# Performance work log

Measured on AMD Instinct MI355X. Metric: run time of the kernel, lower is better.

Reference implementation:

```python
import jax, jax.numpy as jnp
import numpy as np

NUM_USER = 200000
NUM_ITEM = 100000
DIM = 64
NUM_LAYER = 2  # hardcoded in LightGCN.__init__ (lgn_single(..., num_layer=2))
AVG_DEG = 16
N = NUM_USER + NUM_ITEM
E = N * AVG_DEG
BATCH = 16384


def setup_inputs() -> dict:
    key = jax.random.key(0)
    k = jax.random.split(key, 8)
    emb_user = jax.random.normal(k[0], (NUM_USER, DIM), jnp.float32) * 0.05
    emb_item = jax.random.normal(k[1], (NUM_ITEM, DIM), jnp.float32) * 0.05
    # COO sparse normalized adjacency: out[row] += vals * x[col]
    graph_row = jax.random.randint(k[2], (E,), 0, N, dtype=jnp.int32)
    graph_col = jax.random.randint(k[3], (E,), 0, N, dtype=jnp.int32)
    graph_vals = jax.random.uniform(k[4], (E,), jnp.float32) / AVG_DEG
    user_nodes = jax.random.randint(k[5], (BATCH,), 0, NUM_USER, dtype=jnp.int32)
    pos_item_nodes = jax.random.randint(k[6], (BATCH,), 0, NUM_ITEM, dtype=jnp.int32) + NUM_USER
    neg_item_nodes = jax.random.randint(k[7], (BATCH,), 0, NUM_ITEM, dtype=jnp.int32) + NUM_USER
    return {
        "emb_user": emb_user,
        "emb_item": emb_item,
        "graph_vals": graph_vals,
        "graph_row": graph_row,
        "graph_col": graph_col,
        "user_nodes": user_nodes,
        "pos_item_nodes": pos_item_nodes,
        "neg_item_nodes": neg_item_nodes,
    }


def _spmm(vals, row, col, x):
    # torch.sparse.mm(graph, x) with graph in COO form
    return jax.ops.segment_sum(vals[:, None] * x[col], row, num_segments=N)


def reference(emb_user, emb_item, graph_vals, graph_row, graph_col,
              user_nodes, pos_item_nodes, neg_item_nodes):
    # LGN_single.forward: concat, propagate, mean over layer stack
    all_emb = jnp.concatenate([emb_user, emb_item], axis=0)  # [N, D]
    acc = all_emb
    e = all_emb
    for _ in range(NUM_LAYER):
        e = _spmm(graph_vals, graph_row, graph_col, e)
        acc = acc + e
    light_out = acc / (NUM_LAYER + 1)  # mean of stacked embeddings
    # LightGCN.forward: gather + elementwise dot scores
    u = light_out[user_nodes]          # [B, D]
    p = light_out[pos_item_nodes]      # [B, D]
    n = light_out[neg_item_nodes]      # [B, D]
    pos_scores = jnp.sum(u * p, axis=1)
    neg_scores = jnp.sum(u * n, axis=1)
    return jnp.stack([pos_scores, neg_scores])  # [2, B]
```

## Files before the change

### kernel.cpp

```cpp
#include <hip/hip_runtime.h>

#define DIM 64
#define CHUNK 4096
#define MAXNB 512
#define MAXNBLK 2048
#define BSHIFT 10
#define RPB 1024

__device__ __forceinline__ unsigned short f2bf(float f) {
    unsigned int u = __float_as_uint(f);
    return (unsigned short)((u + 0x7FFFu + ((u >> 16) & 1u)) >> 16);
}
__device__ __forceinline__ float4 bf2f4(uint2 g) {
    float4 x;
    x.x = __uint_as_float(g.x << 16);
    x.y = __uint_as_float(g.x & 0xffff0000u);
    x.z = __uint_as_float(g.y << 16);
    x.w = __uint_as_float(g.y & 0xffff0000u);
    return x;
}

__device__ __forceinline__ int blockScan256(int v, int* sh) {
    int t = threadIdx.x;
    sh[t] = v;
    __syncthreads();
    for (int off = 1; off < 256; off <<= 1) {
        int x = (t >= off) ? sh[t - off] : 0;
        __syncthreads();
        sh[t] += x;
        __syncthreads();
    }
    return sh[t];
}


__global__ void conv2_k(const float* __restrict__ u, const float* __restrict__ it,
                        int nu, int ntot, unsigned short* __restrict__ o) {
    int i = blockIdx.x * blockDim.x + threadIdx.x;
    int stride = gridDim.x * blockDim.x;
    int n8 = ntot >> 3;
    for (int t = i; t < n8; t += stride) {
        int e = t * 8;
        const float* src = (e < nu) ? (u + e) : (it + (e - nu));
        float4 x = *(const float4*)src;
        float4 y = *(const float4*)(src + 4);
        uint4 v;
        v.x = (unsigned)f2bf(x.x) | ((unsigned)f2bf(x.y) << 16);
        v.y = (unsigned)f2bf(x.z) | ((unsigned)f2bf(x.w) << 16);
        v.z = (unsigned)f2bf(y.x) | ((unsigned)f2bf(y.y) << 16);
        v.w = (unsigned)f2bf(y.z) | ((unsigned)f2bf(y.w) << 16);
        ((uint4*)o)[t] = v;
    }
}


__global__ void p1a_hist(const int* __restrict__ row, int E, int NB,
                         int* __restrict__ counts) {
    __shared__ int h[MAXNB];
    for (int b = threadIdx.x; b < NB; b += 256) h[b] = 0;
    __syncthreads();
    int base = blockIdx.x * CHUNK;
    int end = min(base + CHUNK, E);
    int vend = base + ((end - base) & ~3);
    for (int i = base + threadIdx.x * 4; i < vend; i += 1024) {
        int4 r = *(const int4*)(row + i);
        atomicAdd(&h[r.x >> BSHIFT], 1);
        atomicAdd(&h[r.y >> BSHIFT], 1);
        atomicAdd(&h[r.z >> BSHIFT], 1);
        atomicAdd(&h[r.w >> BSHIFT], 1);
    }
    for (int i = vend + threadIdx.x; i < end; i += 256) atomicAdd(&h[row[i] >> BSHIFT], 1);
    __syncthreads();
    int blk = blockIdx.x;
    for (int b = threadIdx.x; b < NB; b += 256) counts[(size_t)blk * NB + b] = h[b];
}

__global__ void p1b_scan(int* __restrict__ counts, int NBLK, int NB,
                         int* __restrict__ bucketTotal) {
    int b = blockIdx.x, t = threadIdx.x;
    __shared__ int sh[256];
    int v[8];
    int run = 0;
#pragma unroll
    for (int i = 0; i < 8; i++) {
        int idx = t * 8 + i;
        int c = (idx < NBLK) ? counts[(size_t)idx * NB + b] : 0;
        v[i] = run;
        run += c;
    }
    int inc = blockScan256(run, sh);
    int excl = inc - run;
#pragma unroll
    for (int i = 0; i < 8; i++) {
        int idx = t * 8 + i;
        if (idx < NBLK) counts[(size_t)idx * NB + b] = v[i] + excl;
    }
    if (t == 255) bucketTotal[b] = sh[255];
}

__global__ void p_scan_tot(const int* __restrict__ bucketTotal, int NB,
                           int* __restrict__ bucketStart) {
    int t = threadIdx.x;
    __shared__ int sh[256];
    int v[8];
    int run = 0;
#pragma unroll
    for (int i = 0; i < 8; i++) {
        int idx = t * 8 + i;
        int c = (idx < NB) ? bucketTotal[idx] : 0;
        v[i] = run;
        run += c;
    }
    int inc = blockScan256(run, sh);
    int excl = inc - run;
#pragma unroll
    for (int i = 0; i < 8; i++) {
        int idx = t * 8 + i;
        if (idx < NB) bucketStart[idx] = v[i] + excl;
    }
    if (t == 255) bucketStart[NB] = sh[255];
}

__global__ void p1c_scatter(const int* __restrict__ row, const int* __restrict__ col,
                            const float* __restrict__ vals, int E, int NB,
                            const int* __restrict__ counts, const int* __restrict__ bucketStart,
                            int2* __restrict__ bdata) {
    __shared__ int cur[MAXNB];
    int blk = blockIdx.x;
    for (int b = threadIdx.x; b < NB; b += 256)
        cur[b] = bucketStart[b] + counts[(size_t)blk * NB + b];
    __syncthreads();
    int base = blk * CHUNK;
    int end = min(base + CHUNK, E);
    int vend = base + ((end - base) & ~3);
    for (int i = base + threadIdx.x * 4; i < vend; i += 1024) {
        int4 r = *(const int4*)(row + i);
        int4 c = *(const int4*)(col + i);
        float4 v = *(const float4*)(vals + i);
        int p0 = atomicAdd(&cur[r.x >> BSHIFT], 1);
        int p1 = atomicAdd(&cur[r.y >> BSHIFT], 1);
        int p2 = atomicAdd(&cur[r.z >> BSHIFT], 1);
        int p3 = atomicAdd(&cur[r.w >> BSHIFT], 1);
        bdata[p0] = make_int2(((r.x & (RPB - 1)) << 20) | c.x, __float_as_int(v.x));
        bdata[p1] = make_int2(((r.y & (RPB - 1)) << 20) | c.y, __float_as_int(v.y));
        bdata[p2] = make_int2(((r.z & (RPB - 1)) << 20) | c.z, __float_as_int(v.z));
        bdata[p3] = make_int2(((r.w & (RPB - 1)) << 20) | c.w, __float_as_int(v.w));
    }
    for (int i = vend + threadIdx.x; i < end; i += 256) {
        int r = row[i];
        int p = atomicAdd(&cur[r >> BSHIFT], 1);
        bdata[p] = make_int2(((r & (RPB - 1)) << 20) | col[i], __float_as_int(vals[i]));
    }
}

__global__ void p2_group(const int2* __restrict__ bdata, const int* __restrict__ bucketStart,
                         int NB, int N, int padMask, int padSlop,
                         int* __restrict__ rowStart, int* __restrict__ rowLen,
                         int2* __restrict__ pairs) {
    __shared__ int hist[RPB];
    __shared__ int sh[256];
    __shared__ int cur[RPB];
    int b = blockIdx.x, t = threadIdx.x;
    int s0 = bucketStart[b], s1 = bucketStart[b + 1];
    int pbase = s0 + b * padSlop;
    for (int i = t; i < RPB; i += 256) hist[i] = 0;
    __syncthreads();
    for (int i = s0 + t; i < s1; i += 256)
        atomicAdd(&hist[(bdata[i].x >> 20) & (RPB - 1)], 1);
    __syncthreads();
    int v[4];
    int run = 0;
#pragma unroll
    for (int i = 0; i < 4; i++) {
        int h = hist[t * 4 + i];
        int hp = (h + padMask) & ~padMask;
        v[i] = run;
        run += hp;
    }
    int inc = blockScan256(run, sh);
    int excl = inc - run;
    int ptot = sh[255];
#pragma unroll
    for (int i = 0; i < 4; i++) {
        int r = (b << BSHIFT) + t * 4 + i;
        int st = excl + v[i];
        if (r < N) {
            int h = hist[t * 4 + i];
            rowStart[r] = pbase + st;
            rowLen[r] = (h + padMask) & ~padMask;
        }
        cur[t * 4 + i] = st;
    }
    __syncthreads();
    for (int i = t; i < ptot; i += 256) pairs[pbase + i] = make_int2(0, 0);
    __syncthreads();
    for (int i = s0 + t; i < s1; i += 256) {
        int2 e = bdata[i];
        int rl = (e.x >> 20) & (RPB - 1);
        int pos = atomicAdd(&cur[rl], 1);
        pairs[pbase + pos] = make_int2((e.x & 0xFFFFF) << 7, e.y);
    }
}


__global__ void spmm1_k(const unsigned short* __restrict__ emb16,
                        const int* __restrict__ rowStart, const int* __restrict__ rowLen,
                        const int2* __restrict__ pairs,
                        int n_total, unsigned short* __restrict__ e1) {
    int wave = (blockIdx.x * blockDim.x + threadIdx.x) >> 6;
    int lane = threadIdx.x & 63;
    if (wave >= n_total) return;
    int eg = lane >> 4, dp = lane & 15;
    unsigned off0 = dp * 8u;
    const char* base = (const char*)emb16;
    int len = rowLen[wave];
    const int2* pp = pairs + rowStart[wave];
    float4 a0 = {0.f, 0.f, 0.f, 0.f}, a1 = {0.f, 0.f, 0.f, 0.f};
    float4 a2 = {0.f, 0.f, 0.f, 0.f}, a3 = {0.f, 0.f, 0.f, 0.f};
    int k = 0;
    for (; k + 16 <= len; k += 16) {
        int2 p0 = pp[k + eg];
        int2 p1 = pp[k + 4 + eg];
        int2 p2 = pp[k + 8 + eg];
        int2 p3 = pp[k + 12 + eg];
        uint2 g0 = *(const uint2*)(base + ((unsigned)p0.x + off0));
        uint2 g1 = *(const uint2*)(base + ((unsigned)p1.x + off0));
        uint2 g2 = *(const uint2*)(base + ((unsigned)p2.x + off0));
        uint2 g3 = *(const uint2*)(base + ((unsigned)p3.x + off0));
        float v0 = __int_as_float(p0.y), v1 = __int_as_float(p1.y);
        float v2 = __int_as_float(p2.y), v3 = __int_as_float(p3.y);
        float4 x0 = bf2f4(g0), x1 = bf2f4(g1), x2 = bf2f4(g2), x3 = bf2f4(g3);
        a0.x += v0 * x0.x; a0.y += v0 * x0.y; a0.z += v0 * x0.z; a0.w += v0 * x0.w;
        a1.x += v1 * x1.x; a1.y += v1 * x1.y; a1.z += v1 * x1.z; a1.w += v1 * x1.w;
        a2.x += v2 * x2.x; a2.y += v2 * x2.y; a2.z += v2 * x2.z; a2.w += v2 * x2.w;
        a3.x += v3 * x3.x; a3.y += v3 * x3.y; a3.z += v3 * x3.z; a3.w += v3 * x3.w;
    }
    for (; k < len; k += 8) {
        int2 p0 = pp[k + eg];
        int2 p1 = pp[k + 4 + eg];
        uint2 g0 = *(const uint2*)(base + ((unsigned)p0.x + off0));
        uint2 g1 = *(const uint2*)(base + ((unsigned)p1.x + off0));
        float v0 = __int_as_float(p0.y), v1 = __int_as_float(p1.y);
        float4 x0 = bf2f4(g0), x1 = bf2f4(g1);
        a0.x += v0 * x0.x; a0.y += v0 * x0.y; a0.z += v0 * x0.z; a0.w += v0 * x0.w;
        a1.x += v1 * x1.x; a1.y += v1 * x1.y; a1.z += v1 * x1.z; a1.w += v1 * x1.w;
    }
    float4 s;
    s.x = (a0.x + a1.x) + (a2.x + a3.x);
    s.y = (a0.y + a1.y) + (a2.y + a3.y);
    s.z = (a0.z + a1.z) + (a2.z + a3.z);
    s.w = (a0.w + a1.w) + (a2.w + a3.w);
    s.x += __shfl_xor(s.x, 16); s.y += __shfl_xor(s.y, 16);
    s.z += __shfl_xor(s.z, 16); s.w += __shfl_xor(s.w, 16);
    s.x += __shfl_xor(s.x, 32); s.y += __shfl_xor(s.y, 32);
    s.z += __shfl_xor(s.z, 32); s.w += __shfl_xor(s.w, 32);
    if (eg == 0) {
        uint2 o;
        o.x = (unsigned)f2bf(s.x) | ((unsigned)f2bf(s.y) << 16);
        o.y = (unsigned)f2bf(s.z) | ((unsigned)f2bf(s.w) << 16);
        *(uint2*)(e1 + (size_t)wave * DIM + dp * 4) = o;
    }
}


__global__ void final_k(const float* __restrict__ emb_user, const float* __restrict__ emb_item,
                        int n_user, const unsigned short* __restrict__ e1,
                        const int* __restrict__ rowStart, const int* __restrict__ rowLen,
                        const int2* __restrict__ pairs,
                        const int* __restrict__ u_nodes, const int* __restrict__ p_nodes,
                        const int* __restrict__ n_nodes, int B, float* __restrict__ out) {
    int wave = (blockIdx.x * blockDim.x + threadIdx.x) >> 6;
    int lane = threadIdx.x & 63;
    if (wave >= B) return;
    int eg = lane >> 4, dp = lane & 15;
    unsigned off0 = dp * 8u;
    const char* base = (const char*)e1;
    int nid[3] = {u_nodes[wave], p_nodes[wave], n_nodes[wave]};
    float4 l[3];
#pragma unroll
    for (int j = 0; j < 3; j++) {
        int r = nid[j];
        const float* base0 = (r < n_user) ? (emb_user + (size_t)r * DIM)
                                          : (emb_item + (size_t)(r - n_user) * DIM);
        float4 acc = *(const float4*)(base0 + dp * 4);
        float4 t1 = bf2f4(*(const uint2*)(e1 + (size_t)r * DIM + dp * 4));
        acc.x += t1.x; acc.y += t1.y; acc.z += t1.z; acc.w += t1.w;
        int len = rowLen[r];
        const int2* pp = pairs + rowStart[r];
        float4 a0 = {0.f, 0.f, 0.f, 0.f}, a1 = {0.f, 0.f, 0.f, 0.f};
        float4 a2 = {0.f, 0.f, 0.f, 0.f}, a3 = {0.f, 0.f, 0.f, 0.f};
        int k = 0;
        for (; k + 16 <= len; k += 16) {
            int2 p0 = pp[k + eg];
            int2 p1 = pp[k + 4 + eg];
            int2 p2 = pp[k + 8 + eg];
            int2 p3 = pp[k + 12 + eg];
            uint2 g0 = *(const uint2*)(base + ((unsigned)p0.x + off0));
            uint2 g1 = *(const uint2*)(base + ((unsigned)p1.x + off0));
            uint2 g2 = *(const uint2*)(base + ((unsigned)p2.x + off0));
            uint2 g3 = *(const uint2*)(base + ((unsigned)p3.x + off0));
            float v0 = __int_as_float(p0.y), v1 = __int_as_float(p1.y);
            float v2 = __int_as_float(p2.y), v3 = __int_as_float(p3.y);
            float4 x0 = bf2f4(g0), x1 = bf2f4(g1), x2 = bf2f4(g2), x3 = bf2f4(g3);
            a0.x += v0 * x0.x; a0.y += v0 * x0.y; a0.z += v0 * x0.z; a0.w += v0 * x0.w;
            a1.x += v1 * x1.x; a1.y += v1 * x1.y; a1.z += v1 * x1.z; a1.w += v1 * x1.w;
            a2.x += v2 * x2.x; a2.y += v2 * x2.y; a2.z += v2 * x2.z; a2.w += v2 * x2.w;
            a3.x += v3 * x3.x; a3.y += v3 * x3.y; a3.z += v3 * x3.z; a3.w += v3 * x3.w;
        }
        for (; k < len; k += 8) {
            int2 p0 = pp[k + eg];
            int2 p1 = pp[k + 4 + eg];
            uint2 g0 = *(const uint2*)(base + ((unsigned)p0.x + off0));
            uint2 g1 = *(const uint2*)(base + ((unsigned)p1.x + off0));
            float v0 = __int_as_float(p0.y), v1 = __int_as_float(p1.y);
            float4 x0 = bf2f4(g0), x1 = bf2f4(g1);
            a0.x += v0 * x0.x; a0.y += v0 * x0.y; a0.z += v0 * x0.z; a0.w += v0 * x0.w;
            a1.x += v1 * x1.x; a1.y += v1 * x1.y; a1.z += v1 * x1.z; a1.w += v1 * x1.w;
        }
        float4 s;
        s.x = (a0.x + a1.x) + (a2.x + a3.x);
        s.y = (a0.y + a1.y) + (a2.y + a3.y);
        s.z = (a0.z + a1.z) + (a2.z + a3.z);
        s.w = (a0.w + a1.w) + (a2.w + a3.w);
        s.x += __shfl_xor(s.x, 16); s.y += __shfl_xor(s.y, 16);
        s.z += __shfl_xor(s.z, 16); s.w += __shfl_xor(s.w, 16);
        s.x += __shfl_xor(s.x, 32); s.y += __shfl_xor(s.y, 32);
        s.z += __shfl_xor(s.z, 32); s.w += __shfl_xor(s.w, 32);
        l[j].x = (acc.x + s.x) * (1.0f / 3.0f);
        l[j].y = (acc.y + s.y) * (1.0f / 3.0f);
        l[j].z = (acc.z + s.z) * (1.0f / 3.0f);
        l[j].w = (acc.w + s.w) * (1.0f / 3.0f);
    }
    float ps = l[0].x * l[1].x + l[0].y * l[1].y + l[0].z * l[1].z + l[0].w * l[1].w;
    float ns = l[0].x * l[2].x + l[0].y * l[2].y + l[0].z * l[2].z + l[0].w * l[2].w;
    ps += __shfl_xor(ps, 1); ns += __shfl_xor(ns, 1);
    ps += __shfl_xor(ps, 2); ns += __shfl_xor(ns, 2);
    ps += __shfl_xor(ps, 4); ns += __shfl_xor(ns, 4);
    ps += __shfl_xor(ps, 8); ns += __shfl_xor(ns, 8);
    if (lane == 0) {
        out[wave] = ps;
        out[B + wave] = ns;
    }
}

extern "C" void kernel_launch(void* const* d_in, const int* in_sizes, int n_in,
                              void* d_out, int out_size, void* d_ws, size_t ws_size,
                              hipStream_t stream) {
    const float* emb_user = (const float*)d_in[0];
    const float* emb_item = (const float*)d_in[1];
    const float* gvals    = (const float*)d_in[2];
    const int*   grow     = (const int*)d_in[3];
    const int*   gcol     = (const int*)d_in[4];
    const int*   unodes   = (const int*)d_in[5];
    const int*   pnodes   = (const int*)d_in[6];
    const int*   nnodes   = (const int*)d_in[7];
    float* out = (float*)d_out;

    int n_user = in_sizes[0] / DIM;
    int n_item = in_sizes[1] / DIM;
    int N = n_user + n_item;
    int E = in_sizes[2];
    int B = in_sizes[5];
    int NB = (N + RPB - 1) >> BSHIFT;
    int NBLK = (E + CHUNK - 1) / CHUNK;

    auto align256 = [](size_t x) { return (x + 255) & ~(size_t)255; };
    size_t embBytes = (size_t)N * DIM * 2;
    size_t countsBytes = (size_t)NBLK * NB * 4;
    size_t regionBBytes = (size_t)E * 8 > embBytes ? (size_t)E * 8 : embBytes;
    size_t regionABytes = countsBytes > embBytes ? countsBytes : embBytes;
    size_t fixedBytes = align256((size_t)N * 4) + align256((size_t)N * 4) +
                        align256((size_t)MAXNB * 4) + align256((size_t)(MAXNB + 1) * 4) +
                        align256(regionBBytes) + align256(regionABytes);
    int padMask = 15;
    size_t pairsBytes = ((size_t)E + (size_t)NB * RPB * padMask) * 8;
    if (fixedBytes + align256(pairsBytes) > ws_size) {
        padMask = 7;
        pairsBytes = ((size_t)E + (size_t)NB * RPB * padMask) * 8;
    }
    int padSlop = RPB * padMask;

    char* ws = (char*)d_ws;
    size_t off = 0;
    auto alloc = [&](size_t bytes) -> void* {
        void* p = ws + off;
        off = (off + bytes + 255) & ~(size_t)255;
        return p;
    };
    int*  rowStart    = (int*)alloc((size_t)N * 4);
    int*  rowLen      = (int*)alloc((size_t)N * 4);
    int*  bucketTotal = (int*)alloc((size_t)MAXNB * 4);
    int*  bucketStart = (int*)alloc((size_t)(MAXNB + 1) * 4);
    int2* pairs       = (int2*)alloc(pairsBytes);
    char* regionB = (char*)alloc(regionBBytes);
    int2*           bdata = (int2*)regionB;
    unsigned short* emb16 = (unsigned short*)regionB;
    char* regionA = (char*)alloc(regionABytes);
    int*            counts = (int*)regionA;
    unsigned short* e1     = (unsigned short*)regionA;
    (void)n_in; (void)out_size;

    p1a_hist<<<NBLK, 256, 0, stream>>>(grow, E, NB, counts);
    p1b_scan<<<NB, 256, 0, stream>>>(counts, NBLK, NB, bucketTotal);
    p_scan_tot<<<1, 256, 0, stream>>>(bucketTotal, NB, bucketStart);
    p1c_scatter<<<NBLK, 256, 0, stream>>>(grow, gcol, gvals, E, NB, counts, bucketStart, bdata);
    p2_group<<<NB, 256, 0, stream>>>(bdata, bucketStart, NB, N, padMask, padSlop,
                                     rowStart, rowLen, pairs);

    conv2_k<<<2048, 256, 0, stream>>>(emb_user, emb_item, n_user * DIM, N * DIM, emb16);

    spmm1_k<<<(N + 3) / 4, 256, 0, stream>>>(emb16, rowStart, rowLen, pairs, N, e1);
    final_k<<<(B + 3) / 4, 256, 0, stream>>>(emb_user, emb_item, n_user, e1,
                                             rowStart, rowLen, pairs,
                                             unodes, pnodes, nnodes, B, out);
}
```

Before: 328.8 us.

## Pad rows to 8, zero only pad slots, vectorize pair loads, larger chunks

Fixes the row padding at multiples of 8 as a compile-time constant and drops the workspace-size check. The zero-fill of the whole padded pairs region is replaced by writing zeros only into each row's tail padding after the scatter, which removes a full write pass and one barrier. The SpMM loops now fetch two adjacent (col,val) pairs per lane with one 16-byte load. The histogram/scatter chunk size is doubled, halving the block count and the size of the counts array. The per-row zero loop is serial per thread, and the missing workspace check means a small workspace would now go unnoticed.

```diff
diff --git a/kernel.cpp b/kernel.cpp
--- a/kernel.cpp
+++ b/kernel.cpp
@@ -1,11 +1,11 @@
 #include <hip/hip_runtime.h>
 
 #define DIM 64
-#define CHUNK 4096
+#define CHUNK 8192
 #define MAXNB 512
-#define MAXNBLK 2048
 #define BSHIFT 10
 #define RPB 1024
+#define PADMASK 7
 
 __device__ __forceinline__ unsigned short f2bf(float f) {
     unsigned int u = __float_as_uint(f);
@@ -154,7 +154,7 @@
 }
 
 __global__ void p2_group(const int2* __restrict__ bdata, const int* __restrict__ bucketStart,
-                         int NB, int N, int padMask, int padSlop,
+                         int NB, int N, int padSlop,
                          int* __restrict__ rowStart, int* __restrict__ rowLen,
                          int2* __restrict__ pairs) {
     __shared__ int hist[RPB];
@@ -173,13 +173,12 @@
 #pragma unroll
     for (int i = 0; i < 4; i++) {
         int h = hist[t * 4 + i];
-        int hp = (h + padMask) & ~padMask;
+        int hp = (h + PADMASK) & ~PADMASK;
         v[i] = run;
         run += hp;
     }
     int inc = blockScan256(run, sh);
     int excl = inc - run;
-    int ptot = sh[255];
 #pragma unroll
     for (int i = 0; i < 4; i++) {
         int r = (b << BSHIFT) + t * 4 + i;
@@ -187,18 +186,25 @@
         if (r < N) {
             int h = hist[t * 4 + i];
             rowStart[r] = pbase + st;
-            rowLen[r] = (h + padMask) & ~padMask;
+            rowLen[r] = (h + PADMASK) & ~PADMASK;
         }
         cur[t * 4 + i] = st;
     }
-    __syncthreads();
-    for (int i = t; i < ptot; i += 256) pairs[pbase + i] = make_int2(0, 0);
     __syncthreads();
     for (int i = s0 + t; i < s1; i += 256) {
         int2 e = bdata[i];
         int rl = (e.x >> 20) & (RPB - 1);
         int pos = atomicAdd(&cur[rl], 1);
         pairs[pbase + pos] = make_int2((e.x & 0xFFFFF) << 7, e.y);
+    }
+    __syncthreads();
+#pragma unroll
+    for (int i = 0; i < 4; i++) {
+        int h = hist[t * 4 + i];
+        int hp = (h + PADMASK) & ~PADMASK;
+        int st = excl + v[i];
+        for (int p = st + h; p < st + hp; p++)
+            pairs[pbase + p] = make_int2(0, 0);
     }
 }
 
@@ -219,16 +225,14 @@
     float4 a2 = {0.f, 0.f, 0.f, 0.f}, a3 = {0.f, 0.f, 0.f, 0.f};
     int k = 0;
     for (; k + 16 <= len; k += 16) {
-        int2 p0 = pp[k + eg];
-        int2 p1 = pp[k + 4 + eg];
-        int2 p2 = pp[k + 8 + eg];
-        int2 p3 = pp[k + 12 + eg];
-        uint2 g0 = *(const uint2*)(base + ((unsigned)p0.x + off0));
-        uint2 g1 = *(const uint2*)(base + ((unsigned)p1.x + off0));
-        uint2 g2 = *(const uint2*)(base + ((unsigned)p2.x + off0));
-        uint2 g3 = *(const uint2*)(base + ((unsigned)p3.x + off0));
-        float v0 = __int_as_float(p0.y), v1 = __int_as_float(p1.y);
-        float v2 = __int_as_float(p2.y), v3 = __int_as_float(p3.y);
+        int4 q0 = *(const int4*)(pp + k + 2 * eg);
+        int4 q1 = *(const int4*)(pp + k + 8 + 2 * eg);
+        uint2 g0 = *(const uint2*)(base + ((unsigned)q0.x + off0));
+        uint2 g1 = *(const uint2*)(base + ((unsigned)q0.z + off0));
+        uint2 g2 = *(const uint2*)(base + ((unsigned)q1.x + off0));
+        uint2 g3 = *(const uint2*)(base + ((unsigned)q1.z + off0));
+        float v0 = __int_as_float(q0.y), v1 = __int_as_float(q0.w);
+        float v2 = __int_as_float(q1.y), v3 = __int_as_float(q1.w);
         float4 x0 = bf2f4(g0), x1 = bf2f4(g1), x2 = bf2f4(g2), x3 = bf2f4(g3);
         a0.x += v0 * x0.x; a0.y += v0 * x0.y; a0.z += v0 * x0.z; a0.w += v0 * x0.w;
         a1.x += v1 * x1.x; a1.y += v1 * x1.y; a1.z += v1 * x1.z; a1.w += v1 * x1.w;
@@ -236,11 +240,10 @@
         a3.x += v3 * x3.x; a3.y += v3 * x3.y; a3.z += v3 * x3.z; a3.w += v3 * x3.w;
     }
     for (; k < len; k += 8) {
-        int2 p0 = pp[k + eg];
-        int2 p1 = pp[k + 4 + eg];
-        uint2 g0 = *(const uint2*)(base + ((unsigned)p0.x + off0));
-        uint2 g1 = *(const uint2*)(base + ((unsigned)p1.x + off0));
-        float v0 = __int_as_float(p0.y), v1 = __int_as_float(p1.y);
+        int4 q0 = *(const int4*)(pp + k + 2 * eg);
+        uint2 g0 = *(const uint2*)(base + ((unsigned)q0.x + off0));
+        uint2 g1 = *(const uint2*)(base + ((unsigned)q0.z + off0));
+        float v0 = __int_as_float(q0.y), v1 = __int_as_float(q0.w);
         float4 x0 = bf2f4(g0), x1 = bf2f4(g1);
         a0.x += v0 * x0.x; a0.y += v0 * x0.y; a0.z += v0 * x0.z; a0.w += v0 * x0.w;
         a1.x += v1 * x1.x; a1.y += v1 * x1.y; a1.z += v1 * x1.z; a1.w += v1 * x1.w;
@@ -291,16 +294,14 @@
         float4 a2 = {0.f, 0.f, 0.f, 0.f}, a3 = {0.f, 0.f, 0.f, 0.f};
         int k = 0;
         for (; k + 16 <= len; k += 16) {
-            int2 p0 = pp[k + eg];
-            int2 p1 = pp[k + 4 + eg];
-            int2 p2 = pp[k + 8 + eg];
-            int2 p3 = pp[k + 12 + eg];
-            uint2 g0 = *(const uint2*)(base + ((unsigned)p0.x + off0));
-            uint2 g1 = *(const uint2*)(base + ((unsigned)p1.x + off0));
-            uint2 g2 = *(const uint2*)(base + ((unsigned)p2.x + off0));
-            uint2 g3 = *(const uint2*)(base + ((unsigned)p3.x + off0));
-            float v0 = __int_as_float(p0.y), v1 = __int_as_float(p1.y);
-            float v2 = __int_as_float(p2.y), v3 = __int_as_float(p3.y);
+            int4 q0 = *(const int4*)(pp + k + 2 * eg);
+            int4 q1 = *(const int4*)(pp + k + 8 + 2 * eg);
+            uint2 g0 = *(const uint2*)(base + ((unsigned)q0.x + off0));
+            uint2 g1 = *(const uint2*)(base + ((unsigned)q0.z + off0));
+            uint2 g2 = *(const uint2*)(base + ((unsigned)q1.x + off0));
+            uint2 g3 = *(const uint2*)(base + ((unsigned)q1.z + off0));
+            float v0 = __int_as_float(q0.y), v1 = __int_as_float(q0.w);
+            float v2 = __int_as_float(q1.y), v3 = __int_as_float(q1.w);
             float4 x0 = bf2f4(g0), x1 = bf2f4(g1), x2 = bf2f4(g2), x3 = bf2f4(g3);
             a0.x += v0 * x0.x; a0.y += v0 * x0.y; a0.z += v0 * x0.z; a0.w += v0 * x0.w;
             a1.x += v1 * x1.x; a1.y += v1 * x1.y; a1.z += v1 * x1.z; a1.w += v1 * x1.w;
@@ -308,11 +309,10 @@
             a3.x += v3 * x3.x; a3.y += v3 * x3.y; a3.z += v3 * x3.z; a3.w += v3 * x3.w;
         }
         for (; k < len; k += 8) {
-            int2 p0 = pp[k + eg];
-            int2 p1 = pp[k + 4 + eg];
-            uint2 g0 = *(const uint2*)(base + ((unsigned)p0.x + off0));
-            uint2 g1 = *(const uint2*)(base + ((unsigned)p1.x + off0));
-            float v0 = __int_as_float(p0.y), v1 = __int_as_float(p1.y);
+            int4 q0 = *(const int4*)(pp + k + 2 * eg);
+            uint2 g0 = *(const uint2*)(base + ((unsigned)q0.x + off0));
+            uint2 g1 = *(const uint2*)(base + ((unsigned)q0.z + off0));
+            float v0 = __int_as_float(q0.y), v1 = __int_as_float(q0.w);
             float4 x0 = bf2f4(g0), x1 = bf2f4(g1);
             a0.x += v0 * x0.x; a0.y += v0 * x0.y; a0.z += v0 * x0.z; a0.w += v0 * x0.w;
             a1.x += v1 * x1.x; a1.y += v1 * x1.y; a1.z += v1 * x1.z; a1.w += v1 * x1.w;
@@ -363,22 +363,7 @@
     int B = in_sizes[5];
     int NB = (N + RPB - 1) >> BSHIFT;
     int NBLK = (E + CHUNK - 1) / CHUNK;
-
-    auto align256 = [](size_t x) { return (x + 255) & ~(size_t)255; };
-    size_t embBytes = (size_t)N * DIM * 2;
-    size_t countsBytes = (size_t)NBLK * NB * 4;
-    size_t regionBBytes = (size_t)E * 8 > embBytes ? (size_t)E * 8 : embBytes;
-    size_t regionABytes = countsBytes > embBytes ? countsBytes : embBytes;
-    size_t fixedBytes = align256((size_t)N * 4) + align256((size_t)N * 4) +
-                        align256((size_t)MAXNB * 4) + align256((size_t)(MAXNB + 1) * 4) +
-                        align256(regionBBytes) + align256(regionABytes);
-    int padMask = 15;
-    size_t pairsBytes = ((size_t)E + (size_t)NB * RPB * padMask) * 8;
-    if (fixedBytes + align256(pairsBytes) > ws_size) {
-        padMask = 7;
-        pairsBytes = ((size_t)E + (size_t)NB * RPB * padMask) * 8;
-    }
-    int padSlop = RPB * padMask;
+    int padSlop = RPB * PADMASK;
 
     char* ws = (char*)d_ws;
     size_t off = 0;
@@ -387,6 +372,12 @@
         off = (off + bytes + 255) & ~(size_t)255;
         return p;
     };
+    size_t embBytes = (size_t)N * DIM * 2;
+    size_t countsBytes = (size_t)NBLK * NB * 4;
+    size_t regionBBytes = (size_t)E * 8 > embBytes ? (size_t)E * 8 : embBytes;
+    size_t regionABytes = countsBytes > embBytes ? countsBytes : embBytes;
+    size_t pairsBytes = ((size_t)E + (size_t)NB * padSlop) * 8;
+
     int*  rowStart    = (int*)alloc((size_t)N * 4);
     int*  rowLen      = (int*)alloc((size_t)N * 4);
     int*  bucketTotal = (int*)alloc((size_t)MAXNB * 4);
@@ -398,13 +389,13 @@
     char* regionA = (char*)alloc(regionABytes);
     int*            counts = (int*)regionA;
     unsigned short* e1     = (unsigned short*)regionA;
-    (void)n_in; (void)out_size;
+    (void)n_in; (void)out_size; (void)ws_size;
 
     p1a_hist<<<NBLK, 256, 0, stream>>>(grow, E, NB, counts);
     p1b_scan<<<NB, 256, 0, stream>>>(counts, NBLK, NB, bucketTotal);
     p_scan_tot<<<1, 256, 0, stream>>>(bucketTotal, NB, bucketStart);
     p1c_scatter<<<NBLK, 256, 0, stream>>>(grow, gcol, gvals, E, NB, counts, bucketStart, bdata);
-    p2_group<<<NB, 256, 0, stream>>>(bdata, bucketStart, NB, N, padMask, padSlop,
+    p2_group<<<NB, 256, 0, stream>>>(bdata, bucketStart, NB, N, padSlop,
                                      rowStart, rowLen, pairs);
 
     conv2_k<<<2048, 256, 0, stream>>>(emb_user, emb_item, n_user * DIM, N * DIM, emb16);
```

New measurement: 307.4 us. 6.5% less time.
